# Kernel optimization log

Hardware: AMD Instinct MI355X
Metric: run time of the kernel (lower is better)

Reference implementation:

```python
import jax, jax.numpy as jnp
import numpy as np

B, S, H = 8, 512, 768
NH, KVH, HD = 12, 4, 64
E, TOPK, IE = 8, 2, 1536
EPS = 1e-6
ROPE_THETA = 10000.0


def _rmsnorm(x, w):
    xf = x.astype(jnp.float32)
    var = jnp.mean(xf * xf, axis=-1, keepdims=True)
    return (w * (xf * jax.lax.rsqrt(var + EPS))).astype(x.dtype)


def _rotate_half(x):
    x1, x2 = jnp.split(x, 2, axis=-1)
    return jnp.concatenate((-x2, x1), axis=-1)


def setup_inputs() -> dict:
    key = jax.random.key(0)
    ks = iter(jax.random.split(key, 40))

    def nrm(shape, scale=0.02):
        return jax.random.normal(next(ks), shape, dtype=jnp.float32) * scale

    inp = {}
    inp["hidden_states"] = jax.random.normal(next(ks), (B, S, H), dtype=jnp.float32)
    causal = jnp.tril(jnp.ones((S, S), dtype=bool))
    inp["attention_mask"] = jnp.where(causal, 0.0, -1e9).astype(jnp.float32)[None, None]  # [1,1,S,S]
    inp["group_attention_mask"] = jnp.zeros((S, 1, B, B), dtype=jnp.float32)
    inp["position_ids"] = jnp.broadcast_to(jnp.arange(S, dtype=jnp.int32), (B, S))
    # RMSNorm weights
    inp["ln1_w"] = jnp.ones((H,), jnp.float32)
    inp["ln2_w"] = jnp.ones((H,), jnp.float32)
    inp["ln3_w"] = jnp.ones((H,), jnp.float32)
    # self (time) attention params
    inp["sq_w"] = nrm((NH * HD, H)); inp["sq_b"] = jnp.zeros((NH * HD,), jnp.float32)
    inp["sk_w"] = nrm((KVH * HD, H)); inp["sk_b"] = jnp.zeros((KVH * HD,), jnp.float32)
    inp["sv_w"] = nrm((KVH * HD, H)); inp["sv_b"] = jnp.zeros((KVH * HD,), jnp.float32)
    inp["so_w"] = nrm((H, NH * HD))
    # group (cross-channel) attention params
    inp["gq_w"] = nrm((NH * HD, H)); inp["gq_b"] = jnp.zeros((NH * HD,), jnp.float32)
    inp["gk_w"] = nrm((KVH * HD, H)); inp["gk_b"] = jnp.zeros((KVH * HD,), jnp.float32)
    inp["gv_w"] = nrm((KVH * HD, H)); inp["gv_b"] = jnp.zeros((KVH * HD,), jnp.float32)
    inp["go_w"] = nrm((H, NH * HD))
    # MoE params: router + stacked expert weights
    inp["gate_w"] = nrm((E, H))
    inp["w_gate"] = nrm((E, H, IE))
    inp["w_up"] = nrm((E, H, IE))
    inp["w_down"] = nrm((E, IE, H))
    return inp


def reference(hidden_states, attention_mask, group_attention_mask, position_ids,
              ln1_w, ln2_w, ln3_w,
              sq_w, sq_b, sk_w, sk_b, sv_w, sv_b, so_w,
              gq_w, gq_b, gk_w, gk_b, gv_w, gv_b, go_w,
              gate_w, w_gate, w_up, w_down):
    dtype = hidden_states.dtype
    b, s, h = hidden_states.shape
    rep = NH // KVH
    scale = 1.0 / np.sqrt(HD).astype(np.float32)

    # ---- self attention with RoPE (causal, GQA) ----
    residual = hidden_states
    x = _rmsnorm(hidden_states, ln1_w)
    q = (x @ sq_w.T + sq_b).reshape(b, s, NH, HD).transpose(0, 2, 1, 3)   # [b,n,s,d]
    k = (x @ sk_w.T + sk_b).reshape(b, s, KVH, HD).transpose(0, 2, 1, 3)
    v = (x @ sv_w.T + sv_b).reshape(b, s, KVH, HD).transpose(0, 2, 1, 3)
    inv_freq = 1.0 / (ROPE_THETA ** (jnp.arange(0, HD, 2, dtype=jnp.float32) / HD))
    freqs = position_ids.astype(jnp.float32)[..., None] * inv_freq        # [b,s,d/2]
    emb = jnp.concatenate((freqs, freqs), axis=-1)
    cos = jnp.cos(emb)[:, None].astype(dtype)                             # [b,1,s,d]
    sin = jnp.sin(emb)[:, None].astype(dtype)
    q = q * cos + _rotate_half(q) * sin
    k = k * cos + _rotate_half(k) * sin
    k = jnp.repeat(k, rep, axis=1)
    v = jnp.repeat(v, rep, axis=1)
    scores = jnp.einsum('bnqd,bnkd->bnqk', q, k) * scale + attention_mask
    probs = jax.nn.softmax(scores.astype(jnp.float32), axis=-1).astype(dtype)
    attn = jnp.einsum('bnqk,bnkd->bnqd', probs, v)
    attn = attn.transpose(0, 2, 1, 3).reshape(b, s, h) @ so_w.T
    hidden_states = residual + attn

    # ---- group attention: MHA across channels (batch dim), no RoPE ----
    residual = hidden_states
    xg = _rmsnorm(hidden_states, ln2_w).transpose(1, 0, 2)                # [s,b,h]
    q = (xg @ gq_w.T + gq_b).reshape(s, b, NH, HD).transpose(0, 2, 1, 3)  # [s,n,b,d]
    k = (xg @ gk_w.T + gk_b).reshape(s, b, KVH, HD).transpose(0, 2, 1, 3)
    v = (xg @ gv_w.T + gv_b).reshape(s, b, KVH, HD).transpose(0, 2, 1, 3)
    k = jnp.repeat(k, rep, axis=1)
    v = jnp.repeat(v, rep, axis=1)
    gsc = jnp.einsum('snbd,sncd->snbc', q, k) * scale + group_attention_mask
    gpr = jax.nn.softmax(gsc.astype(jnp.float32), axis=-1).astype(dtype)
    ga = jnp.einsum('snbc,sncd->snbd', gpr, v)                            # [s,n,b,d]
    ga = ga.transpose(0, 2, 1, 3).reshape(s, b, h) @ go_w.T               # [s,b,h]
    hidden_states = residual + ga.transpose(1, 0, 2)

    # ---- sparse MoE FFN (top-k routing, weights NOT renormalized) ----
    residual = hidden_states
    xf = _rmsnorm(hidden_states, ln3_w).reshape(b * s, h)                 # [T,h]
    logits = xf @ gate_w.T                                                # [T,E]
    routing = jax.nn.softmax(logits.astype(jnp.float32), axis=-1)
    topw, topi = jax.lax.top_k(routing, TOPK)
    combine = jnp.zeros((b * s, E), jnp.float32).at[
        jnp.arange(b * s)[:, None], topi].set(topw)                        # [T,E]
    out = jnp.zeros_like(xf)
    for e in range(E):  # fixed small expert count; each iter is a grouped GEMM
        ge = jax.nn.silu(xf @ w_gate[e]) * (xf @ w_up[e])                 # [T,IE]
        out = out + combine[:, e:e + 1].astype(dtype) * (ge @ w_down[e])
    hidden_states = residual + out.reshape(b, s, h)
    return hidden_states
```

## Files before the change

### kernel.cpp

```cpp
#include <hip/hip_runtime.h>
#include <math.h>

#define BATCH 8
#define SEQ 512
#define HID 768
#define NHEAD 12
#define KVHEAD 4
#define HDIM 64
#define NEXP 8
#define TOPK 2
#define IEXP 1536
#define NTOK (BATCH * SEQ)
#define NSLOT (NTOK * TOPK)
#define REP (NHEAD / KVHEAD)
#define KVD (KVHEAD * HDIM)

typedef unsigned short u16;
typedef float f32x4 __attribute__((ext_vector_type(4)));
typedef __bf16 bf16x8 __attribute__((ext_vector_type(8)));
typedef unsigned short u16x8 __attribute__((ext_vector_type(8)));

__device__ __forceinline__ u16 f2bf(float f) {
    unsigned u = __float_as_uint(f);
    u += 0x7fffu + ((u >> 16) & 1u);
    return (u16)(u >> 16);
}
__device__ __forceinline__ float bf2f(u16 h) {
    return __uint_as_float(((unsigned)h) << 16);
}

__device__ __forceinline__ void gload16(const void* g, void* l) {
    __builtin_amdgcn_global_load_lds(
        (const __attribute__((address_space(1))) void*)g,
        (__attribute__((address_space(3))) void*)l, 16, 0, 0);
}

__device__ __forceinline__ void cvt8(float4 a, float4 b, u16x8& hi, u16x8& lo) {
    float x[8] = {a.x, a.y, a.z, a.w, b.x, b.y, b.z, b.w};
#pragma unroll
    for (int i = 0; i < 8; ++i) {
        u16 h = f2bf(x[i]);
        hi[i] = h;
        lo[i] = f2bf(x[i] - bf2f(h));
    }
}

#define SW(row, col) (((row) << 6) + ((col) ^ (((row) & 7) << 3)))

__global__ __launch_bounds__(256)
void cvt_split8(const float* __restrict__ sq, const float* __restrict__ sk,
                const float* __restrict__ sv, const float* __restrict__ so,
                const float* __restrict__ gq, const float* __restrict__ gk,
                const float* __restrict__ gv, const float* __restrict__ go,
                u16* __restrict__ wqs_h, u16* __restrict__ wqs_l,
                u16* __restrict__ wos_h, u16* __restrict__ wos_l,
                u16* __restrict__ wqg_h, u16* __restrict__ wqg_l,
                u16* __restrict__ wog_h, u16* __restrict__ wog_l) {
    int i4 = (blockIdx.x * 256 + threadIdx.x) * 4;
    const float* src;
    u16 *dh, *dl;
    int s;
    if (i4 < 983040) {
        dh = wqs_h; dl = wqs_l;
        if (i4 < 589824)      { src = sq; s = i4; }
        else if (i4 < 786432) { src = sk; s = i4 - 589824; dh += 589824; dl += 589824; }
        else                  { src = sv; s = i4 - 786432; dh += 786432; dl += 786432; }
    } else if (i4 < 1572864) {
        src = so; s = i4 - 983040; dh = wos_h; dl = wos_l;
    } else if (i4 < 2555904) {
        int j = i4 - 1572864;
        dh = wqg_h; dl = wqg_l;
        if (j < 589824)      { src = gq; s = j; }
        else if (j < 786432) { src = gk; s = j - 589824; dh += 589824; dl += 589824; }
        else                 { src = gv; s = j - 786432; dh += 786432; dl += 786432; }
    } else {
        src = go; s = i4 - 2555904; dh = wog_h; dl = wog_l;
    }
    float4 v = *(const float4*)(src + s);
    float a[4] = {v.x, v.y, v.z, v.w};
    ushort4 h, lo;
    u16 t;
    t = f2bf(a[0]); h.x = t; lo.x = f2bf(a[0] - bf2f(t));
    t = f2bf(a[1]); h.y = t; lo.y = f2bf(a[1] - bf2f(t));
    t = f2bf(a[2]); h.z = t; lo.z = f2bf(a[2] - bf2f(t));
    t = f2bf(a[3]); h.w = t; lo.w = f2bf(a[3] - bf2f(t));
    *(ushort4*)(dh + s) = h;
    *(ushort4*)(dl + s) = lo;
}

__global__ __launch_bounds__(256)
void transpose_cvt(const float* __restrict__ src, u16* __restrict__ dst,
                   int R, int C) {
    const int e = blockIdx.z;
    src += (size_t)e * R * C;
    dst += (size_t)e * R * C;
    __shared__ float t[32][33];
    const int c0 = blockIdx.x << 5, r0 = blockIdx.y << 5;
    const int tx = threadIdx.x, ty = threadIdx.y;
#pragma unroll
    for (int i = 0; i < 4; ++i)
        t[ty * 4 + i][tx] = src[(size_t)(r0 + ty * 4 + i) * C + c0 + tx];
    __syncthreads();
#pragma unroll
    for (int i = 0; i < 4; ++i)
        dst[(size_t)(c0 + ty * 4 + i) * R + r0 + tx] = f2bf(t[tx][ty * 4 + i]);
}

__global__ __launch_bounds__(256)
void rmsnorm_split(const float* __restrict__ X, const float* __restrict__ W,
                   u16* __restrict__ Yh, u16* __restrict__ Yl) {
    const int t = blockIdx.x;
    const int tid = threadIdx.x;
    const float* x = X + (size_t)t * HID;
    float x0 = x[tid], x1 = x[tid + 256], x2 = x[tid + 512];
    float ss = x0 * x0 + x1 * x1 + x2 * x2;
    for (int m = 1; m < 64; m <<= 1) ss += __shfl_xor(ss, m);
    __shared__ float red[4];
    if ((tid & 63) == 0) red[tid >> 6] = ss;
    __syncthreads();
    float tot = red[0] + red[1] + red[2] + red[3];
    float inv = rsqrtf(tot * (1.0f / HID) + 1e-6f);
    u16* yh = Yh + (size_t)t * HID;
    u16* yl = Yl + (size_t)t * HID;
#pragma unroll
    for (int j = 0; j < 3; ++j) {
        int idx = tid + j * 256;
        float r = x[idx] * inv * W[idx];
        u16 h = f2bf(r);
        yh[idx] = h;
        yl[idx] = f2bf(r - bf2f(h));
    }
}

__global__ __launch_bounds__(256)
void rmsnorm_kernel(const float* __restrict__ X, const float* __restrict__ W,
                    float* __restrict__ Y, u16* __restrict__ Ybf) {
    const int t = blockIdx.x;
    const int tid = threadIdx.x;
    const float* x = X + (size_t)t * HID;
    float x0 = x[tid], x1 = x[tid + 256], x2 = x[tid + 512];
    float ss = x0 * x0 + x1 * x1 + x2 * x2;
    for (int m = 1; m < 64; m <<= 1) ss += __shfl_xor(ss, m);
    __shared__ float red[4];
    if ((tid & 63) == 0) red[tid >> 6] = ss;
    __syncthreads();
    float tot = red[0] + red[1] + red[2] + red[3];
    float inv = rsqrtf(tot * (1.0f / HID) + 1e-6f);
    float r0 = x0 * inv * W[tid];
    float r1 = x1 * inv * W[tid + 256];
    float r2 = x2 * inv * W[tid + 512];
    float* y = Y + (size_t)t * HID;
    y[tid] = r0; y[tid + 256] = r1; y[tid + 512] = r2;
    u16* yb = Ybf + (size_t)t * HID;
    yb[tid] = f2bf(r0); yb[tid + 256] = f2bf(r1); yb[tid + 512] = f2bf(r2);
}

__global__ __launch_bounds__(256)
void qkv_split(const u16* __restrict__ Xh, const u16* __restrict__ Xl,
               const u16* __restrict__ Wh, const u16* __restrict__ Wl,
               const float* __restrict__ bq, const float* __restrict__ bk,
               const float* __restrict__ bv,
               u16* __restrict__ Qh, u16* __restrict__ Ql,
               u16* __restrict__ Kh, u16* __restrict__ Kl,
               float* __restrict__ Vo) {
    __shared__ __align__(16) u16 Ah[4096], Al[4096], Bh[4096], Bl[4096];
    const int tid = threadIdx.x, l = tid & 63, w = tid >> 6;
    const int wm = w & 1, wn = w >> 1;
    const int m0 = blockIdx.y << 7, n0 = blockIdx.x << 7;
    const int sr = l >> 2, sc8 = (l & 3) << 3;
    const u16* gAh0 = Xh + (size_t)(m0 + w * 32 + sr) * HID + sc8;
    const u16* gAh1 = gAh0 + 16 * HID;
    const u16* gAl0 = Xl + (size_t)(m0 + w * 32 + sr) * HID + sc8;
    const u16* gAl1 = gAl0 + 16 * HID;
    const u16* gBh0 = Wh + (size_t)(n0 + w * 32 + sr) * HID + sc8;
    const u16* gBh1 = gBh0 + 16 * HID;
    const u16* gBl0 = Wl + (size_t)(n0 + w * 32 + sr) * HID + sc8;
    const u16* gBl1 = gBl0 + 16 * HID;
    u16* lAh0 = Ah + w * 1024; u16* lAh1 = lAh0 + 512;
    u16* lAl0 = Al + w * 1024; u16* lAl1 = lAl0 + 512;
    u16* lBh0 = Bh + w * 1024; u16* lBh1 = lBh0 + 512;
    u16* lBl0 = Bl + w * 1024; u16* lBl1 = lBl0 + 512;
    const int fr = l & 15, fc = (l >> 4) << 3;
    f32x4 acc[4][4];
#pragma unroll
    for (int i = 0; i < 4; ++i)
#pragma unroll
        for (int j = 0; j < 4; ++j) acc[i][j] = (f32x4){0.f, 0.f, 0.f, 0.f};
    for (int k0 = 0; k0 < HID; k0 += 32) {
        gload16(gAh0 + k0, lAh0);
        gload16(gAh1 + k0, lAh1);
        gload16(gAl0 + k0, lAl0);
        gload16(gAl1 + k0, lAl1);
        gload16(gBh0 + k0, lBh0);
        gload16(gBh1 + k0, lBh1);
        gload16(gBl0 + k0, lBl0);
        gload16(gBl1 + k0, lBl1);
        __syncthreads();
        bf16x8 ah[4], al[4], bh[4], bl[4];
#pragma unroll
        for (int i = 0; i < 4; ++i) {
            ah[i] = *(const bf16x8*)(Ah + (wm * 64 + i * 16 + fr) * 32 + fc);
            al[i] = *(const bf16x8*)(Al + (wm * 64 + i * 16 + fr) * 32 + fc);
            bh[i] = *(const bf16x8*)(Bh + (wn * 64 + i * 16 + fr) * 32 + fc);
            bl[i] = *(const bf16x8*)(Bl + (wn * 64 + i * 16 + fr) * 32 + fc);
        }
#pragma unroll
        for (int mf = 0; mf < 4; ++mf)
#pragma unroll
            for (int nf = 0; nf < 4; ++nf) {
                acc[mf][nf] = __builtin_amdgcn_mfma_f32_16x16x32_bf16(
                    ah[mf], bh[nf], acc[mf][nf], 0, 0, 0);
                acc[mf][nf] = __builtin_amdgcn_mfma_f32_16x16x32_bf16(
                    al[mf], bh[nf], acc[mf][nf], 0, 0, 0);
                acc[mf][nf] = __builtin_amdgcn_mfma_f32_16x16x32_bf16(
                    ah[mf], bl[nf], acc[mf][nf], 0, 0, 0);
            }
        __syncthreads();
    }
    const int er = (l >> 4) << 2, ec = l & 15;
    if (n0 < 1024) {
        u16 *oh, *olo; const float* bp; int ldc, nl;
        if (n0 < 768) { oh = Qh; olo = Ql; bp = bq; ldc = 768; nl = n0; }
        else          { oh = Kh; olo = Kl; bp = bk; ldc = KVD; nl = n0 - 768; }
#pragma unroll
        for (int mf = 0; mf < 4; ++mf)
#pragma unroll
            for (int i = 0; i < 4; ++i) {
                int row = m0 + wm * 64 + mf * 16 + er + i;
#pragma unroll
                for (int nf = 0; nf < 4; ++nf) {
                    int col = nl + wn * 64 + nf * 16 + ec;
                    float v = acc[mf][nf][i] + bp[col];
                    size_t idx = (size_t)row * ldc + col;
                    u16 h = f2bf(v);
                    oh[idx] = h;
                    olo[idx] = f2bf(v - bf2f(h));
                }
            }
    } else {
        int nl = n0 - 1024;
#pragma unroll
        for (int mf = 0; mf < 4; ++mf)
#pragma unroll
            for (int i = 0; i < 4; ++i) {
                int row = m0 + wm * 64 + mf * 16 + er + i;
#pragma unroll
                for (int nf = 0; nf < 4; ++nf) {
                    int col = nl + wn * 64 + nf * 16 + ec;
                    Vo[(size_t)row * KVD + col] = acc[mf][nf][i] + bv[col];
                }
            }
    }
}

__global__ __launch_bounds__(256)
void oproj_split(const u16* __restrict__ Ahg, const u16* __restrict__ Alg,
                 const u16* __restrict__ Wh, const u16* __restrict__ Wl,
                 const float* __restrict__ resid, float* __restrict__ C,
                 int M, int N, int K) {
    __shared__ __align__(16) u16 Ah[4096], Al[4096], Bh[4096], Bl[4096];
    const int tid = threadIdx.x, l = tid & 63, w = tid >> 6;
    const int wm = w & 1, wn = w >> 1;
    const int m0 = blockIdx.y << 7, n0 = blockIdx.x << 7;
    const int sr = l >> 2, sc8 = (l & 3) << 3;
    const u16* gAh0 = Ahg + (size_t)(m0 + w * 32 + sr) * K + sc8;
    const u16* gAh1 = gAh0 + (size_t)16 * K;
    const u16* gAl0 = Alg + (size_t)(m0 + w * 32 + sr) * K + sc8;
    const u16* gAl1 = gAl0 + (size_t)16 * K;
    const u16* gBh0 = Wh + (size_t)(n0 + w * 32 + sr) * K + sc8;
    const u16* gBh1 = gBh0 + (size_t)16 * K;
    const u16* gBl0 = Wl + (size_t)(n0 + w * 32 + sr) * K + sc8;
    const u16* gBl1 = gBl0 + (size_t)16 * K;
    u16* lAh0 = Ah + w * 1024; u16* lAh1 = lAh0 + 512;
    u16* lAl0 = Al + w * 1024; u16* lAl1 = lAl0 + 512;
    u16* lBh0 = Bh + w * 1024; u16* lBh1 = lBh0 + 512;
    u16* lBl0 = Bl + w * 1024; u16* lBl1 = lBl0 + 512;
    const int fr = l & 15, fc = (l >> 4) << 3;
    f32x4 acc[4][4];
#pragma unroll
    for (int i = 0; i < 4; ++i)
#pragma unroll
        for (int j = 0; j < 4; ++j) acc[i][j] = (f32x4){0.f, 0.f, 0.f, 0.f};
    for (int k0 = 0; k0 < K; k0 += 32) {
        gload16(gAh0 + k0, lAh0);
        gload16(gAh1 + k0, lAh1);
        gload16(gAl0 + k0, lAl0);
        gload16(gAl1 + k0, lAl1);
        gload16(gBh0 + k0, lBh0);
        gload16(gBh1 + k0, lBh1);
        gload16(gBl0 + k0, lBl0);
        gload16(gBl1 + k0, lBl1);
        __syncthreads();
        bf16x8 ah[4], al[4], bh[4], bl[4];
#pragma unroll
        for (int i = 0; i < 4; ++i) {
            ah[i] = *(const bf16x8*)(Ah + (wm * 64 + i * 16 + fr) * 32 + fc);
            al[i] = *(const bf16x8*)(Al + (wm * 64 + i * 16 + fr) * 32 + fc);
            bh[i] = *(const bf16x8*)(Bh + (wn * 64 + i * 16 + fr) * 32 + fc);
            bl[i] = *(const bf16x8*)(Bl + (wn * 64 + i * 16 + fr) * 32 + fc);
        }
#pragma unroll
        for (int mf = 0; mf < 4; ++mf)
#pragma unroll
            for (int nf = 0; nf < 4; ++nf) {
                acc[mf][nf] = __builtin_amdgcn_mfma_f32_16x16x32_bf16(
                    ah[mf], bh[nf], acc[mf][nf], 0, 0, 0);
                acc[mf][nf] = __builtin_amdgcn_mfma_f32_16x16x32_bf16(
                    al[mf], bh[nf], acc[mf][nf], 0, 0, 0);
                acc[mf][nf] = __builtin_amdgcn_mfma_f32_16x16x32_bf16(
                    ah[mf], bl[nf], acc[mf][nf], 0, 0, 0);
            }
        __syncthreads();
    }
    const int er = (l >> 4) << 2, ec = l & 15;
#pragma unroll
    for (int mf = 0; mf < 4; ++mf)
#pragma unroll
        for (int i = 0; i < 4; ++i) {
            int row = m0 + wm * 64 + mf * 16 + er + i;
#pragma unroll
            for (int nf = 0; nf < 4; ++nf) {
                int col = n0 + wn * 64 + nf * 16 + ec;
                C[(size_t)row * N + col] =
                    acc[mf][nf][i] + resid[(size_t)row * N + col];
            }
        }
}

__global__ __launch_bounds__(256)
void rope_split(u16* __restrict__ Qh, u16* __restrict__ Ql,
                u16* __restrict__ Kh, u16* __restrict__ Kl,
                const int* __restrict__ pos_ids) {
    const int t = blockIdx.x;
    const float pos = (float)pos_ids[t];
    const int tid = threadIdx.x;
#pragma unroll
    for (int it = 0; it < 2; ++it) {
        int p = tid + (it << 8);
        int head = p >> 5, i = p & 31;
        float invf = expf(-(float)i * 0.28782313662425572f);
        float ang = pos * invf;
        float c = cosf(ang), sn = sinf(ang);
        u16 *ah, *al;
        size_t bofs;
        if (head < NHEAD) { ah = Qh; al = Ql; bofs = (size_t)t * HID + head * HDIM; }
        else { ah = Kh; al = Kl; bofs = (size_t)t * KVD + (head - NHEAD) * HDIM; }
        float x1 = bf2f(ah[bofs + i]) + bf2f(al[bofs + i]);
        float x2 = bf2f(ah[bofs + i + 32]) + bf2f(al[bofs + i + 32]);
        float y1 = x1 * c - x2 * sn;
        float y2 = x2 * c + x1 * sn;
        u16 h1 = f2bf(y1);
        ah[bofs + i] = h1;
        al[bofs + i] = f2bf(y1 - bf2f(h1));
        u16 h2 = f2bf(y2);
        ah[bofs + i + 32] = h2;
        al[bofs + i + 32] = f2bf(y2 - bf2f(h2));
    }
}

__global__ __launch_bounds__(256)
void attn_self_mfma(const u16* __restrict__ Qhg, const u16* __restrict__ Qlg,
                    const u16* __restrict__ Khg, const u16* __restrict__ Klg,
                    const float* __restrict__ V,
                    u16* __restrict__ Oh, u16* __restrict__ Ol) {
    const int qt = blockIdx.x, n = blockIdx.y, b = blockIdx.z;
    const int kv = n / REP;
    const int tid = threadIdx.x, l = tid & 63, w = tid >> 6;
    const int q0 = qt << 5;
    __shared__ __align__(16) u16 sQh[2048], sQl[2048];
    __shared__ __align__(16) u16 sKh[4096], sKl[4096];
    __shared__ __align__(16) u16 sVh[4096], sVl[4096];
    __shared__ float Ps[32][68];
    __shared__ float scal[32];

    {
        int row = tid >> 3, cg = (tid & 7) << 3;
        size_t gq = (size_t)(b * SEQ + q0 + row) * HID + n * HDIM + cg;
        *(u16x8*)(sQh + SW(row, cg)) = *(const u16x8*)(Qhg + gq);
        *(u16x8*)(sQl + SW(row, cg)) = *(const u16x8*)(Qlg + gq);
    }
    __syncthreads();

    const int fr = l & 15, fcg = (l >> 4) << 3;
    const int qf16 = (w & 1) << 4;
    const int fp2 = (w >> 1) << 1;
    bf16x8 qfh[2], qfl[2];
#pragma unroll
    for (int dc = 0; dc < 2; ++dc) {
        int off = SW(qf16 + fr, dc * 32 + fcg);
        qfh[dc] = *(const bf16x8*)(sQh + off);
        qfl[dc] = *(const bf16x8*)(sQl + off);
    }

    f32x4 o[2];
    o[0] = (f32x4){0.f, 0.f, 0.f, 0.f};
    o[1] = (f32x4){0.f, 0.f, 0.f, 0.f};
    float m_run = -3.4e38f, l_run = 0.f;
    const int sq = tid >> 3;
    const int skb = (tid & 7) << 3;
    const float scale = 0.125f;
    const int nt = (qt >> 1) + 1;

    for (int t = 0; t < nt; ++t) {
        __syncthreads();
        {
            int row = tid >> 2, cg = (tid & 3) << 4;
            size_t gk = (size_t)(b * SEQ + (t << 6) + row) * KVD + kv * HDIM + cg;
            *(u16x8*)(sKh + SW(row, cg))     = *(const u16x8*)(Khg + gk);
            *(u16x8*)(sKh + SW(row, cg + 8)) = *(const u16x8*)(Khg + gk + 8);
            *(u16x8*)(sKl + SW(row, cg))     = *(const u16x8*)(Klg + gk);
            *(u16x8*)(sKl + SW(row, cg + 8)) = *(const u16x8*)(Klg + gk + 8);
        }
        {
            int kp = (tid & 31) << 1, dc = (tid >> 5) << 3;
            const float* vg0 = V + (size_t)(b * SEQ + (t << 6) + kp) * KVD
                               + kv * HDIM + dc;
            const float* vg1 = vg0 + KVD;
            float4 a0 = *(const float4*)vg0;
            float4 a1 = *(const float4*)(vg0 + 4);
            float4 b0 = *(const float4*)vg1;
            float4 b1 = *(const float4*)(vg1 + 4);
            float va[8] = {a0.x, a0.y, a0.z, a0.w, a1.x, a1.y, a1.z, a1.w};
            float vb[8] = {b0.x, b0.y, b0.z, b0.w, b1.x, b1.y, b1.z, b1.w};
#pragma unroll
            for (int j = 0; j < 8; ++j) {
                u16 h0 = f2bf(va[j]);
                u16 h1 = f2bf(vb[j]);
                u16 p0 = f2bf(va[j] - bf2f(h0));
                u16 p1 = f2bf(vb[j] - bf2f(h1));
                int off = SW(dc + j, kp);
                *(unsigned*)(sVh + off) = (unsigned)h0 | ((unsigned)h1 << 16);
                *(unsigned*)(sVl + off) = (unsigned)p0 | ((unsigned)p1 << 16);
            }
        }
        __syncthreads();
#pragma unroll
        for (int kk = 0; kk < 2; ++kk) {
            int kf = fp2 + kk;
            bf16x8 kh[2], klv[2];
#pragma unroll
            for (int dc = 0; dc < 2; ++dc) {
                int off = SW(kf * 16 + fr, dc * 32 + fcg);
                kh[dc]  = *(const bf16x8*)(sKh + off);
                klv[dc] = *(const bf16x8*)(sKl + off);
            }
            f32x4 s = (f32x4){0.f, 0.f, 0.f, 0.f};
            s = __builtin_amdgcn_mfma_f32_16x16x32_bf16(qfh[0], kh[0], s, 0, 0, 0);
            s = __builtin_amdgcn_mfma_f32_16x16x32_bf16(qfh[1], kh[1], s, 0, 0, 0);
            s = __builtin_amdgcn_mfma_f32_16x16x32_bf16(qfl[0], kh[0], s, 0, 0, 0);
            s = __builtin_amdgcn_mfma_f32_16x16x32_bf16(qfl[1], kh[1], s, 0, 0, 0);
            s = __builtin_amdgcn_mfma_f32_16x16x32_bf16(qfh[0], klv[0], s, 0, 0, 0);
            s = __builtin_amdgcn_mfma_f32_16x16x32_bf16(qfh[1], klv[1], s, 0, 0, 0);
            int col = kf * 16 + fr;
            int key = (t << 6) + col;
#pragma unroll
            for (int r = 0; r < 4; ++r) {
                int qrow = qf16 + ((l >> 4) << 2) + r;
                Ps[qrow][col] = (key <= q0 + qrow) ? s[r] * scale : -1e9f;
            }
        }
        __syncthreads();
        {
            float4 s0 = *(const float4*)&Ps[sq][skb];
            float4 s1 = *(const float4*)&Ps[sq][skb + 4];
            float sv[8] = {s0.x, s0.y, s0.z, s0.w, s1.x, s1.y, s1.z, s1.w};
            float mx = sv[0];
#pragma unroll
            for (int j = 1; j < 8; ++j) mx = fmaxf(mx, sv[j]);
            for (int x = 1; x < 8; x <<= 1) mx = fmaxf(mx, __shfl_xor(mx, x));
            float mnew = fmaxf(m_run, mx);
            float corr = __expf(m_run - mnew);
            float lsum = 0.f;
#pragma unroll
            for (int j = 0; j < 8; ++j) {
                sv[j] = __expf(sv[j] - mnew);
                lsum += sv[j];
            }
            for (int x = 1; x < 8; x <<= 1) lsum += __shfl_xor(lsum, x);
            l_run = l_run * corr + lsum;
            m_run = mnew;
            *(float4*)&Ps[sq][skb]     = make_float4(sv[0], sv[1], sv[2], sv[3]);
            *(float4*)&Ps[sq][skb + 4] = make_float4(sv[4], sv[5], sv[6], sv[7]);
            if ((tid & 7) == 0) scal[sq] = corr;
        }
        __syncthreads();
        {
            float4 c4 = *(const float4*)&scal[qf16 + ((l >> 4) << 2)];
            float cr[4] = {c4.x, c4.y, c4.z, c4.w};
#pragma unroll
            for (int dfi = 0; dfi < 2; ++dfi)
#pragma unroll
                for (int r = 0; r < 4; ++r) o[dfi][r] *= cr[r];
            bf16x8 ph[2], pl[2];
#pragma unroll
            for (int kc = 0; kc < 2; ++kc) {
                float4 p0 = *(const float4*)&Ps[qf16 + fr][kc * 32 + fcg];
                float4 p1 = *(const float4*)&Ps[qf16 + fr][kc * 32 + fcg + 4];
                u16x8 hh, ll;
                cvt8(p0, p1, hh, ll);
                ph[kc] = *(bf16x8*)&hh;
                pl[kc] = *(bf16x8*)&ll;
            }
#pragma unroll
            for (int dfi = 0; dfi < 2; ++dfi) {
                int df = fp2 + dfi;
#pragma unroll
                for (int kc = 0; kc < 2; ++kc) {
                    int off = SW(df * 16 + fr, kc * 32 + fcg);
                    bf16x8 vh = *(const bf16x8*)(sVh + off);
                    bf16x8 vl = *(const bf16x8*)(sVl + off);
                    o[dfi] = __builtin_amdgcn_mfma_f32_16x16x32_bf16(
                        ph[kc], vh, o[dfi], 0, 0, 0);
                    o[dfi] = __builtin_amdgcn_mfma_f32_16x16x32_bf16(
                        pl[kc], vh, o[dfi], 0, 0, 0);
                    o[dfi] = __builtin_amdgcn_mfma_f32_16x16x32_bf16(
                        ph[kc], vl, o[dfi], 0, 0, 0);
                }
            }
        }
    }
    __syncthreads();
    if ((tid & 7) == 0) scal[sq] = 1.0f / l_run;
    __syncthreads();
    {
        int qrb = qf16 + ((l >> 4) << 2);
        float4 li4 = *(const float4*)&scal[qrb];
        float li[4] = {li4.x, li4.y, li4.z, li4.w};
#pragma unroll
        for (int dfi = 0; dfi < 2; ++dfi) {
            int df = fp2 + dfi;
            int col = n * HDIM + df * 16 + fr;
#pragma unroll
            for (int r = 0; r < 4; ++r) {
                int row = q0 + qrb + r;
                float val = o[dfi][r] * li[r];
                size_t oidx = (size_t)(b * SEQ + row) * HID + col;
                u16 h = f2bf(val);
                Oh[oidx] = h;
                Ol[oidx] = f2bf(val - bf2f(h));
            }
        }
    }
}

__global__ __launch_bounds__(64)
void attn_group(const u16* __restrict__ Qh, const u16* __restrict__ Ql,
                const u16* __restrict__ Kh, const u16* __restrict__ Kl,
                const float* __restrict__ V, const float* __restrict__ gmask,
                u16* __restrict__ Oh, u16* __restrict__ Ol) {
    const int n = blockIdx.x % NHEAD;
    const int s = blockIdx.x / NHEAD;
    const int kv = n / REP;
    const int lane = threadIdx.x;
    __shared__ float Qs[8][65], Ks[8][65], Vs[8][65], Ps[64];
    for (int c = 0; c < 8; ++c) {
        size_t qi = (size_t)(c * SEQ + s) * HID + n * HDIM + lane;
        size_t ki = (size_t)(c * SEQ + s) * KVD + kv * HDIM + lane;
        Qs[c][lane] = bf2f(Qh[qi]) + bf2f(Ql[qi]);
        Ks[c][lane] = bf2f(Kh[ki]) + bf2f(Kl[ki]);
        Vs[c][lane] = V[ki];
    }
    __syncthreads();
    const int qb = lane >> 3, kb = lane & 7;
    float sc = 0;
    for (int d = 0; d < 64; ++d) sc += Qs[qb][d] * Ks[kb][d];
    sc = sc * 0.125f + gmask[(size_t)s * 64 + qb * 8 + kb];
    float m = sc;
    for (int x = 1; x < 8; x <<= 1) m = fmaxf(m, __shfl_xor(m, x));
    float p = __expf(sc - m);
    float l = p;
    for (int x = 1; x < 8; x <<= 1) l += __shfl_xor(l, x);
    Ps[lane] = p / l;
    __syncthreads();
    for (int q2 = 0; q2 < 8; ++q2) {
        float o = 0;
        for (int c = 0; c < 8; ++c) o += Ps[q2 * 8 + c] * Vs[c][lane];
        size_t oidx = (size_t)(q2 * SEQ + s) * HID + n * HDIM + lane;
        u16 h = f2bf(o);
        Oh[oidx] = h;
        Ol[oidx] = f2bf(o - bf2f(h));
    }
}

__global__ __launch_bounds__(64)
void router_kernel(const float* __restrict__ X, const float* __restrict__ GW,
                   int* __restrict__ counts, int* __restrict__ topi,
                   float* __restrict__ topw, int* __restrict__ posb) {
    const int t = blockIdx.x;
    const int lane = threadIdx.x;
    const int e = lane >> 3, c = lane & 7;
    const float4* x4 = (const float4*)(X + (size_t)t * HID + c * 96);
    const float4* g4 = (const float4*)(GW + (size_t)e * HID + c * 96);
    float p = 0;
#pragma unroll
    for (int i = 0; i < 24; ++i) {
        float4 xv = x4[i], gv = g4[i];
        p += xv.x * gv.x + xv.y * gv.y + xv.z * gv.z + xv.w * gv.w;
    }
    p += __shfl_xor(p, 1);
    p += __shfl_xor(p, 2);
    p += __shfl_xor(p, 4);
    float lg[8];
#pragma unroll
    for (int i = 0; i < 8; ++i) lg[i] = __shfl(p, i * 8);
    float m = lg[0];
#pragma unroll
    for (int i = 1; i < 8; ++i) m = fmaxf(m, lg[i]);
    float s = 0;
#pragma unroll
    for (int i = 0; i < 8; ++i) { lg[i] = expf(lg[i] - m); s += lg[i]; }
    float inv = 1.0f / s;
    int i1 = 0; float b1 = lg[0];
#pragma unroll
    for (int i = 1; i < 8; ++i) if (lg[i] > b1) { b1 = lg[i]; i1 = i; }
    int i2 = -1; float b2 = -1.0f;
#pragma unroll
    for (int i = 0; i < 8; ++i)
        if (i != i1 && lg[i] > b2) { b2 = lg[i]; i2 = i; }
    if (lane == 0) {
        topi[t * 2] = i1; topi[t * 2 + 1] = i2;
        topw[t * 2] = b1 * inv; topw[t * 2 + 1] = b2 * inv;
        posb[t * 2] = atomicAdd(&counts[i1], 1);
        posb[t * 2 + 1] = atomicAdd(&counts[i2], 1);
    }
}

__global__ void scan_kernel(const int* __restrict__ counts, int* __restrict__ offsets) {
    int acc = 0;
    for (int e = 0; e < NEXP; ++e) { offsets[e] = acc; acc += counts[e]; }
}

__global__ __launch_bounds__(256)
void fill_slots(const int* __restrict__ topi, const float* __restrict__ topw,
                const int* __restrict__ posb, const int* __restrict__ offsets,
                int* __restrict__ slot_token, float* __restrict__ slot_w,
                int* __restrict__ token_slot) {
    int t = blockIdx.x * 256 + threadIdx.x;
    if (t >= NTOK) return;
#pragma unroll
    for (int k = 0; k < TOPK; ++k) {
        int e = topi[t * 2 + k];
        int sl = offsets[e] + posb[t * 2 + k];
        slot_token[sl] = t;
        slot_w[sl] = topw[t * 2 + k];
        token_slot[t * 2 + k] = sl;
    }
}

__global__ __launch_bounds__(256)
void moe_gate_up(const u16* __restrict__ Xb, const u16* __restrict__ Wg,
                 const u16* __restrict__ Wu,
                 const int* __restrict__ slot_token,
                 const int* __restrict__ counts,
                 const int* __restrict__ offsets, u16* __restrict__ H) {
    const int bid = blockIdx.x;
    const int xcd = bid & 7;
    const int rest = bid >> 3;
    const int mblk = rest & 31;
    const int pg = rest >> 5;
    const int pid = pg * 8 + xcd;
    const int e = pid / 12;
    const int n0 = (pid % 12) << 7;
    const int Ce = counts[e];
    const int m0 = mblk << 7;
    if (Ce == 0 || m0 >= Ce) return;
    const int base = offsets[e];
    __shared__ __align__(16) u16 As[8192];
    __shared__ __align__(16) u16 Gs[8192];
    __shared__ __align__(16) u16 Us[8192];
    const int tid = threadIdx.x, l = tid & 63, w = tid >> 6;
    const int wm = w & 1, wn = w >> 1;
    const int sr = l >> 2, sc8 = (l & 3) << 3;
    int r0 = m0 + w * 32 + sr;
    int r1 = r0 + 16;
    int t0 = slot_token[base + min(r0, Ce - 1)];
    int t1 = slot_token[base + min(r1, Ce - 1)];
    const u16* gA0 = Xb + (size_t)t0 * HID + sc8;
    const u16* gA1 = Xb + (size_t)t1 * HID + sc8;
    const u16* Wge = Wg + (size_t)e * IEXP * HID;
    const u16* Wue = Wu + (size_t)e * IEXP * HID;
    const u16* gG0 = Wge + (size_t)(n0 + w * 32 + sr) * HID + sc8;
    const u16* gG1 = gG0 + 16 * HID;
    const u16* gU0 = Wue + (size_t)(n0 + w * 32 + sr) * HID + sc8;
    const u16* gU1 = gU0 + 16 * HID;
    u16* lA0 = As + w * 1024; u16* lA1 = lA0 + 512;
    u16* lG0 = Gs + w * 1024; u16* lG1 = lG0 + 512;
    u16* lU0 = Us + w * 1024; u16* lU1 = lU0 + 512;
    const int fr = l & 15, fc = (l >> 4) << 3;
    f32x4 accg[4][4], accu[4][4];
#pragma unroll
    for (int i = 0; i < 4; ++i)
#pragma unroll
        for (int j = 0; j < 4; ++j) {
            accg[i][j] = (f32x4){0.f, 0.f, 0.f, 0.f};
            accu[i][j] = (f32x4){0.f, 0.f, 0.f, 0.f};
        }
    for (int k0 = 0; k0 < HID; k0 += 64) {
        gload16(gA0 + k0, lA0);
        gload16(gA1 + k0, lA1);
        gload16(gG0 + k0, lG0);
        gload16(gG1 + k0, lG1);
        gload16(gU0 + k0, lU0);
        gload16(gU1 + k0, lU1);
        gload16(gA0 + k0 + 32, lA0 + 4096);
        gload16(gA1 + k0 + 32, lA1 + 4096);
        gload16(gG0 + k0 + 32, lG0 + 4096);
        gload16(gG1 + k0 + 32, lG1 + 4096);
        gload16(gU0 + k0 + 32, lU0 + 4096);
        gload16(gU1 + k0 + 32, lU1 + 4096);
        __syncthreads();
#pragma unroll
        for (int ks = 0; ks < 2; ++ks) {
            const u16* Ab = As + ks * 4096;
            const u16* Gb = Gs + ks * 4096;
            const u16* Ub = Us + ks * 4096;
            bf16x8 af[4], gf[4], uf[4];
#pragma unroll
            for (int i = 0; i < 4; ++i) {
                af[i] = *(const bf16x8*)(Ab + (wm * 64 + i * 16 + fr) * 32 + fc);
                gf[i] = *(const bf16x8*)(Gb + (wn * 64 + i * 16 + fr) * 32 + fc);
                uf[i] = *(const bf16x8*)(Ub + (wn * 64 + i * 16 + fr) * 32 + fc);
            }
#pragma unroll
            for (int mf = 0; mf < 4; ++mf)
#pragma unroll
                for (int nf = 0; nf < 4; ++nf) {
                    accg[mf][nf] = __builtin_amdgcn_mfma_f32_16x16x32_bf16(
                        af[mf], gf[nf], accg[mf][nf], 0, 0, 0);
                    accu[mf][nf] = __builtin_amdgcn_mfma_f32_16x16x32_bf16(
                        af[mf], uf[nf], accu[mf][nf], 0, 0, 0);
                }
        }
        __syncthreads();
    }
    const int er = (l >> 4) << 2, ec = l & 15;
#pragma unroll
    for (int mf = 0; mf < 4; ++mf)
#pragma unroll
        for (int i = 0; i < 4; ++i) {
            int row = m0 + wm * 64 + mf * 16 + er + i;
            if (row >= Ce) continue;
            size_t sl = (size_t)(base + row);
#pragma unroll
            for (int nf = 0; nf < 4; ++nf) {
                int col = n0 + wn * 64 + nf * 16 + ec;
                float g = accg[mf][nf][i];
                float u = accu[mf][nf][i];
                float h = g / (1.0f + __expf(-g)) * u;
                H[sl * IEXP + col] = f2bf(h);
            }
        }
}

__global__ __launch_bounds__(256)
void moe_down_bf16(const u16* __restrict__ Hb, const u16* __restrict__ Wd,
                   const float* __restrict__ slot_w,
                   const int* __restrict__ counts,
                   const int* __restrict__ offsets, float* __restrict__ D) {
    const int bid = blockIdx.x;
    const int xcd = bid & 7;
    const int rest = bid >> 3;
    const int mblk = rest & 31;
    const int pg = rest >> 5;
    const int pid = pg * 8 + xcd;
    const int e = pid / 6;
    const int n0 = (pid % 6) << 7;
    const int Ce = counts[e];
    const int m0 = mblk << 7;
    if (Ce == 0 || m0 >= Ce) return;
    const int base = offsets[e];
    __shared__ __align__(16) u16 As[8192];
    __shared__ __align__(16) u16 Bs[8192];
    const int tid = threadIdx.x, l = tid & 63, w = tid >> 6;
    const int wm = w & 1, wn = w >> 1;
    const int sr = l >> 2, sc = (l & 3) << 3;
    const u16* Ae = Hb + (size_t)base * IEXP;
    int r0 = min(m0 + w * 32 + sr, Ce - 1);
    int r1 = min(m0 + w * 32 + 16 + sr, Ce - 1);
    const u16* gA0 = Ae + (size_t)r0 * IEXP + sc;
    const u16* gA1 = Ae + (size_t)r1 * IEXP + sc;
    const u16* Wde = Wd + (size_t)e * HID * IEXP;
    const u16* gB0 = Wde + (size_t)(n0 + w * 32 + sr) * IEXP + sc;
    const u16* gB1 = gB0 + 16 * IEXP;
    u16* lA0 = As + w * 1024; u16* lA1 = lA0 + 512;
    u16* lB0 = Bs + w * 1024; u16* lB1 = lB0 + 512;
    const int fr = l & 15, fc = (l >> 4) << 3;
    f32x4 acc[4][4];
#pragma unroll
    for (int i = 0; i < 4; ++i)
#pragma unroll
        for (int j = 0; j < 4; ++j) acc[i][j] = (f32x4){0.f, 0.f, 0.f, 0.f};
    for (int k0 = 0; k0 < IEXP; k0 += 64) {
        gload16(gA0 + k0, lA0);
        gload16(gA1 + k0, lA1);
        gload16(gB0 + k0, lB0);
        gload16(gB1 + k0, lB1);
        gload16(gA0 + k0 + 32, lA0 + 4096);
        gload16(gA1 + k0 + 32, lA1 + 4096);
        gload16(gB0 + k0 + 32, lB0 + 4096);
        gload16(gB1 + k0 + 32, lB1 + 4096);
        __syncthreads();
#pragma unroll
        for (int ks = 0; ks < 2; ++ks) {
            const u16* Ab = As + ks * 4096;
            const u16* Bb = Bs + ks * 4096;
            bf16x8 af[4], bfv[4];
#pragma unroll
            for (int i = 0; i < 4; ++i) {
                af[i]  = *(const bf16x8*)(Ab + (wm * 64 + i * 16 + fr) * 32 + fc);
                bfv[i] = *(const bf16x8*)(Bb + (wn * 64 + i * 16 + fr) * 32 + fc);
            }
#pragma unroll
            for (int mf = 0; mf < 4; ++mf)
#pragma unroll
                for (int nf = 0; nf < 4; ++nf)
                    acc[mf][nf] = __builtin_amdgcn_mfma_f32_16x16x32_bf16(
                        af[mf], bfv[nf], acc[mf][nf], 0, 0, 0);
        }
        __syncthreads();
    }
    const int er = (l >> 4) << 2, ec = l & 15;
#pragma unroll
    for (int mf = 0; mf < 4; ++mf)
#pragma unroll
        for (int i = 0; i < 4; ++i) {
            int row = m0 + wm * 64 + mf * 16 + er + i;
            if (row >= Ce) continue;
            size_t sl = (size_t)(base + row);
            float sw = slot_w[sl];
#pragma unroll
            for (int nf = 0; nf < 4; ++nf) {
                int col = n0 + wn * 64 + nf * 16 + ec;
                D[sl * HID + col] = acc[mf][nf][i] * sw;
            }
        }
}

__global__ __launch_bounds__(256)
void moe_add(float* __restrict__ out, const float* __restrict__ D,
             const int* __restrict__ token_slot) {
    const int t = blockIdx.y;
    const int h = blockIdx.x * 256 + threadIdx.x;
    int s0 = token_slot[t * 2], s1 = token_slot[t * 2 + 1];
    out[(size_t)t * HID + h] += D[(size_t)s0 * HID + h] + D[(size_t)s1 * HID + h];
}

extern "C" void kernel_launch(void* const* d_in, const int* in_sizes, int n_in,
                              void* d_out, int out_size, void* d_ws, size_t ws_size,
                              hipStream_t stream) {
    const float* hidden = (const float*)d_in[0];
    const float* amask  = (const float*)d_in[1];
    const float* gmask  = (const float*)d_in[2];
    const int*   posids = (const int*)d_in[3];
    const float* ln1 = (const float*)d_in[4];
    const float* ln2 = (const float*)d_in[5];
    const float* ln3 = (const float*)d_in[6];
    const float* sqw = (const float*)d_in[7];  const float* sqb = (const float*)d_in[8];
    const float* skw = (const float*)d_in[9];  const float* skb = (const float*)d_in[10];
    const float* svw = (const float*)d_in[11]; const float* svb = (const float*)d_in[12];
    const float* sow = (const float*)d_in[13];
    const float* gqw = (const float*)d_in[14]; const float* gqb = (const float*)d_in[15];
    const float* gkw = (const float*)d_in[16]; const float* gkb = (const float*)d_in[17];
    const float* gvw = (const float*)d_in[18]; const float* gvb = (const float*)d_in[19];
    const float* gow = (const float*)d_in[20];
    const float* gatew = (const float*)d_in[21];
    const float* wg = (const float*)d_in[22];
    const float* wu = (const float*)d_in[23];
    const float* wd = (const float*)d_in[24];
    float* out = (float*)d_out;
    (void)amask;

    char* base = (char*)d_ws;
    u16* xh   = (u16*)(base + 0);
    u16* xl   = (u16*)(base + 6291456);
    u16* qh   = (u16*)(base + 12582912);
    u16* ql   = (u16*)(base + 18874368);
    u16* kh   = (u16*)(base + 25165824);
    u16* kl   = (u16*)(base + 27262976);
    float* vbuf = (float*)(base + 29360128);
    u16* oh   = (u16*)(base + 33554432);
    u16* ol   = (u16*)(base + 39845888);
    u16* wqkv_sh = (u16*)(base + 46137344);
    u16* wqkv_sl = (u16*)(base + 48103424);
    u16* wo_sh   = (u16*)(base + 50069504);
    u16* wo_sl   = (u16*)(base + 51249152);
    u16* wqkv_gh = (u16*)(base + 52428800);
    u16* wqkv_gl = (u16*)(base + 54394880);
    u16* wo_gh   = (u16*)(base + 56360960);
    u16* wo_gl   = (u16*)(base + 57540608);
    u16* wgt = (u16*)(base + 58720256);
    u16* wut = (u16*)(base + 77594624);
    u16* wdt = (u16*)(base + 96468992);
    float* slotw = (float*)(base + 115343360);
    float* topw  = (float*)(base + 115376128);
    int* counts  = (int*)(base + 115408896);
    int* offsets = (int*)(base + 115409024);
    int* topi    = (int*)(base + 115409408);
    int* posb    = (int*)(base + 115442176);
    int* slot_token = (int*)(base + 115474944);
    int* token_slot = (int*)(base + 115507712);
    u16* xbf = (u16*)(base + 115540480);
    float* xb   = (float*)(base + 0);
    u16*   Hbuf = (u16*)(base + 12582912);
    float* Dbuf = (float*)(base + 37748736);

    cvt_split8<<<3072, 256, 0, stream>>>(sqw, skw, svw, sow, gqw, gkw, gvw, gow,
                                         wqkv_sh, wqkv_sl, wo_sh, wo_sl,
                                         wqkv_gh, wqkv_gl, wo_gh, wo_gl);
    transpose_cvt<<<dim3(48, 24, 8), dim3(32, 8), 0, stream>>>(wg, wgt, HID, IEXP);
    transpose_cvt<<<dim3(48, 24, 8), dim3(32, 8), 0, stream>>>(wu, wut, HID, IEXP);
    transpose_cvt<<<dim3(24, 48, 8), dim3(32, 8), 0, stream>>>(wd, wdt, IEXP, HID);

    rmsnorm_split<<<NTOK, 256, 0, stream>>>(hidden, ln1, xh, xl);
    qkv_split<<<dim3(10, 32), 256, 0, stream>>>(xh, xl, wqkv_sh, wqkv_sl,
                                                sqb, skb, svb,
                                                qh, ql, kh, kl, vbuf);
    rope_split<<<NTOK, 256, 0, stream>>>(qh, ql, kh, kl, posids);
    attn_self_mfma<<<dim3(SEQ / 32, NHEAD, BATCH), 256, 0, stream>>>(
        qh, ql, kh, kl, vbuf, oh, ol);
    oproj_split<<<dim3(6, 32), 256, 0, stream>>>(oh, ol, wo_sh, wo_sl,
                                                 hidden, out, NTOK, HID, HID);

    rmsnorm_split<<<NTOK, 256, 0, stream>>>(out, ln2, xh, xl);
    qkv_split<<<dim3(10, 32), 256, 0, stream>>>(xh, xl, wqkv_gh, wqkv_gl,
                                                gqb, gkb, gvb,
                                                qh, ql, kh, kl, vbuf);
    attn_group<<<SEQ * NHEAD, 64, 0, stream>>>(qh, ql, kh, kl, vbuf, gmask,
                                               oh, ol);
    oproj_split<<<dim3(6, 32), 256, 0, stream>>>(oh, ol, wo_gh, wo_gl,
                                                 out, out, NTOK, HID, HID);

    rmsnorm_kernel<<<NTOK, 256, 0, stream>>>(out, ln3, xb, xbf);
    hipMemsetAsync(counts, 0, 8 * sizeof(int), stream);
    router_kernel<<<NTOK, 64, 0, stream>>>(xb, gatew, counts, topi, topw, posb);
    scan_kernel<<<1, 1, 0, stream>>>(counts, offsets);
    fill_slots<<<16, 256, 0, stream>>>(topi, topw, posb, offsets,
                                       slot_token, slotw, token_slot);
    moe_gate_up<<<3072, 256, 0, stream>>>(
        xbf, wgt, wut, slot_token, counts, offsets, Hbuf);
    moe_down_bf16<<<1536, 256, 0, stream>>>(
        Hbuf, wdt, slotw, counts, offsets, Dbuf);
    moe_add<<<dim3(3, NTOK), 256, 0, stream>>>(out, Dbuf, token_slot);
}
```

Measured before the change: 560.7 us.

## Fuse RoPE into QKV GEMM epilogue and widen self-attention query tile

RoPE is now applied inside the QKV projection epilogue, using the fact that each lane holds column pairs i and i+32 in fragments nf and nf+2. This removes the separate rope_split kernel and its read-modify-write of the split Q/K buffers. Separately, self-attention now uses 64-query tiles with 512 threads instead of 32 queries with 256, so each loaded K/V tile serves twice as many queries. The cost is more shared memory per block, fewer blocks, and coarser causal work imbalance.

```diff
diff --git a/kernel.cpp b/kernel.cpp
--- a/kernel.cpp
+++ b/kernel.cpp
@@ -160,6 +160,7 @@
                const u16* __restrict__ Wh, const u16* __restrict__ Wl,
                const float* __restrict__ bq, const float* __restrict__ bk,
                const float* __restrict__ bv,
+               const int* __restrict__ pos_ids, int do_rope,
                u16* __restrict__ Qh, u16* __restrict__ Ql,
                u16* __restrict__ Kh, u16* __restrict__ Kl,
                float* __restrict__ Vo) {
@@ -227,14 +228,30 @@
 #pragma unroll
             for (int i = 0; i < 4; ++i) {
                 int row = m0 + wm * 64 + mf * 16 + er + i;
+                float v[4];
+#pragma unroll
+                for (int nf = 0; nf < 4; ++nf)
+                    v[nf] = acc[mf][nf][i] + bp[nl + wn * 64 + nf * 16 + ec];
+                if (do_rope) {
+                    float pos = (float)pos_ids[row];
+#pragma unroll
+                    for (int p = 0; p < 2; ++p) {
+                        int ii = p * 16 + ec;
+                        float invf = expf(-(float)ii * 0.28782313662425572f);
+                        float ang = pos * invf;
+                        float c = cosf(ang), s = sinf(ang);
+                        float x1 = v[p], x2 = v[p + 2];
+                        v[p]     = x1 * c - x2 * s;
+                        v[p + 2] = x2 * c + x1 * s;
+                    }
+                }
 #pragma unroll
                 for (int nf = 0; nf < 4; ++nf) {
                     int col = nl + wn * 64 + nf * 16 + ec;
-                    float v = acc[mf][nf][i] + bp[col];
                     size_t idx = (size_t)row * ldc + col;
-                    u16 h = f2bf(v);
+                    u16 h = f2bf(v[nf]);
                     oh[idx] = h;
-                    olo[idx] = f2bf(v - bf2f(h));
+                    olo[idx] = f2bf(v[nf] - bf2f(h));
                 }
             }
     } else {
@@ -327,38 +344,7 @@
         }
 }
 
-__global__ __launch_bounds__(256)
-void rope_split(u16* __restrict__ Qh, u16* __restrict__ Ql,
-                u16* __restrict__ Kh, u16* __restrict__ Kl,
-                const int* __restrict__ pos_ids) {
-    const int t = blockIdx.x;
-    const float pos = (float)pos_ids[t];
-    const int tid = threadIdx.x;
-#pragma unroll
-    for (int it = 0; it < 2; ++it) {
-        int p = tid + (it << 8);
-        int head = p >> 5, i = p & 31;
-        float invf = expf(-(float)i * 0.28782313662425572f);
-        float ang = pos * invf;
-        float c = cosf(ang), sn = sinf(ang);
-        u16 *ah, *al;
-        size_t bofs;
-        if (head < NHEAD) { ah = Qh; al = Ql; bofs = (size_t)t * HID + head * HDIM; }
-        else { ah = Kh; al = Kl; bofs = (size_t)t * KVD + (head - NHEAD) * HDIM; }
-        float x1 = bf2f(ah[bofs + i]) + bf2f(al[bofs + i]);
-        float x2 = bf2f(ah[bofs + i + 32]) + bf2f(al[bofs + i + 32]);
-        float y1 = x1 * c - x2 * sn;
-        float y2 = x2 * c + x1 * sn;
-        u16 h1 = f2bf(y1);
-        ah[bofs + i] = h1;
-        al[bofs + i] = f2bf(y1 - bf2f(h1));
-        u16 h2 = f2bf(y2);
-        ah[bofs + i + 32] = h2;
-        al[bofs + i + 32] = f2bf(y2 - bf2f(h2));
-    }
-}
-
-__global__ __launch_bounds__(256)
+__global__ __launch_bounds__(512)
 void attn_self_mfma(const u16* __restrict__ Qhg, const u16* __restrict__ Qlg,
                     const u16* __restrict__ Khg, const u16* __restrict__ Klg,
                     const float* __restrict__ V,
@@ -366,12 +352,12 @@
     const int qt = blockIdx.x, n = blockIdx.y, b = blockIdx.z;
     const int kv = n / REP;
     const int tid = threadIdx.x, l = tid & 63, w = tid >> 6;
-    const int q0 = qt << 5;
-    __shared__ __align__(16) u16 sQh[2048], sQl[2048];
+    const int q0 = qt << 6;
+    __shared__ __align__(16) u16 sQh[4096], sQl[4096];
     __shared__ __align__(16) u16 sKh[4096], sKl[4096];
     __shared__ __align__(16) u16 sVh[4096], sVl[4096];
-    __shared__ float Ps[32][68];
-    __shared__ float scal[32];
+    __shared__ float Ps[64][68];
+    __shared__ float scal[64];
 
     {
         int row = tid >> 3, cg = (tid & 7) << 3;
@@ -382,8 +368,8 @@
     __syncthreads();
 
     const int fr = l & 15, fcg = (l >> 4) << 3;
-    const int qf16 = (w & 1) << 4;
-    const int fp2 = (w >> 1) << 1;
+    const int qf16 = (w & 3) << 4;
+    const int fp2 = (w >> 2) << 1;
     bf16x8 qfh[2], qfl[2];
 #pragma unroll
     for (int dc = 0; dc < 2; ++dc) {
@@ -399,19 +385,17 @@
     const int sq = tid >> 3;
     const int skb = (tid & 7) << 3;
     const float scale = 0.125f;
-    const int nt = (qt >> 1) + 1;
+    const int nt = qt + 1;
 
     for (int t = 0; t < nt; ++t) {
         __syncthreads();
         {
-            int row = tid >> 2, cg = (tid & 3) << 4;
+            int row = tid >> 3, cg = (tid & 7) << 3;
             size_t gk = (size_t)(b * SEQ + (t << 6) + row) * KVD + kv * HDIM + cg;
-            *(u16x8*)(sKh + SW(row, cg))     = *(const u16x8*)(Khg + gk);
-            *(u16x8*)(sKh + SW(row, cg + 8)) = *(const u16x8*)(Khg + gk + 8);
-            *(u16x8*)(sKl + SW(row, cg))     = *(const u16x8*)(Klg + gk);
-            *(u16x8*)(sKl + SW(row, cg + 8)) = *(const u16x8*)(Klg + gk + 8);
-        }
-        {
+            *(u16x8*)(sKh + SW(row, cg)) = *(const u16x8*)(Khg + gk);
+            *(u16x8*)(sKl + SW(row, cg)) = *(const u16x8*)(Klg + gk);
+        }
+        if (tid < 256) {
             int kp = (tid & 31) << 1, dc = (tid >> 5) << 3;
             const float* vg0 = V + (size_t)(b * SEQ + (t << 6) + kp) * KVD
                                + kv * HDIM + dc;
@@ -913,17 +897,16 @@
 
     rmsnorm_split<<<NTOK, 256, 0, stream>>>(hidden, ln1, xh, xl);
     qkv_split<<<dim3(10, 32), 256, 0, stream>>>(xh, xl, wqkv_sh, wqkv_sl,
-                                                sqb, skb, svb,
+                                                sqb, skb, svb, posids, 1,
                                                 qh, ql, kh, kl, vbuf);
-    rope_split<<<NTOK, 256, 0, stream>>>(qh, ql, kh, kl, posids);
-    attn_self_mfma<<<dim3(SEQ / 32, NHEAD, BATCH), 256, 0, stream>>>(
+    attn_self_mfma<<<dim3(SEQ / 64, NHEAD, BATCH), 512, 0, stream>>>(
         qh, ql, kh, kl, vbuf, oh, ol);
     oproj_split<<<dim3(6, 32), 256, 0, stream>>>(oh, ol, wo_sh, wo_sl,
                                                  hidden, out, NTOK, HID, HID);
 
     rmsnorm_split<<<NTOK, 256, 0, stream>>>(out, ln2, xh, xl);
     qkv_split<<<dim3(10, 32), 256, 0, stream>>>(xh, xl, wqkv_gh, wqkv_gl,
-                                                gqb, gkb, gvb,
+                                                gqb, gkb, gvb, posids, 0,
                                                 qh, ql, kh, kl, vbuf);
     attn_group<<<SEQ * NHEAD, 64, 0, stream>>>(qh, ql, kh, kl, vbuf, gmask,
                                                oh, ol);
```

Result: slower. 597.3 us (+6.5%).
